# Kernel tuning notes

Hardware: AMD Instinct MI355X
Metric: run time of the kernel (lower is better)

## Reference

```python
import jax, jax.numpy as jnp
import numpy as np

B, S, D, H = 4, 2048, 512, 8
NEG_INF = -1e9


def setup_inputs() -> dict:
    key = jax.random.key(0)
    ks = jax.random.split(key, 5)
    x = jax.random.normal(ks[0], (B, S, D), dtype=jnp.float32)
    mask = jnp.ones((B, S), dtype=jnp.int32)
    sc = 0.04  # ~1/sqrt(D) init scale
    Wq = jax.random.normal(ks[1], (H, D, D), dtype=jnp.float32) * sc
    Wk = jax.random.normal(ks[2], (H, D, D), dtype=jnp.float32) * sc
    Wv = jax.random.normal(ks[3], (H, D, D), dtype=jnp.float32) * sc
    Wp = jax.random.normal(ks[4], (D, H * D), dtype=jnp.float32) * sc
    return {"x": x, "mask": mask, "Wq": Wq, "Wk": Wk, "Wv": Wv, "Wp": Wp}


def reference(x, mask, Wq, Wk, Wv, Wp):
    d = x.shape[-1]
    scale = 1.0 / jnp.sqrt(jnp.asarray(d, dtype=jnp.float32))
    # torch Linear: y = x @ W.T ; per-head full-width projections
    q = jnp.einsum("bsd,hed->bhse", x, Wq)  # [B,H,S,D]
    k = jnp.einsum("bsd,hed->bhse", x, Wk)
    v = jnp.einsum("bsd,hed->bhse", x, Wv)
    logits = jnp.einsum("bhse,bhte->bhst", q, k) * scale  # [B,H,S,S]
    # pairwise mask = outer product mask[:,:,None] @ mask[:,None,:]
    pair = (mask[:, :, None] * mask[:, None, :])[:, None, :, :]  # [B,1,S,S]
    logits = jnp.where(pair > 0, logits, NEG_INF)
    attn = jax.nn.softmax(logits, axis=-1)
    out = jnp.einsum("bhst,bhte->bhse", attn, v)  # [B,H,S,D]
    # concat heads along last dim (head order preserved) then proj (no bias)
    bsz, h, s, dd = out.shape
    cat = jnp.transpose(out, (0, 2, 1, 3)).reshape(bsz, s, h * dd)
    return jnp.einsum("bsf,df->bsd", cat, Wp)
```

## Files before the change

### kernel.cpp

```cpp
#include <hip/hip_runtime.h>
#include <hip/hip_bf16.h>


using bf16x8 = __attribute__((ext_vector_type(8))) short;
using f32x4  = __attribute__((ext_vector_type(4))) float;
typedef unsigned short u16;

__device__ __forceinline__ u16 f2bf(float f) {
  union { float f; unsigned u; } c; c.f = f;
  unsigned r = c.u + 0x7fffu + ((c.u >> 16) & 1u);
  return (u16)(r >> 16);
}

__device__ __forceinline__ void gload16(const void* g, void* l) {
  __builtin_amdgcn_global_load_lds((const __attribute__((address_space(1))) unsigned int*)g,
                                   (__attribute__((address_space(3))) unsigned int*)l, 16, 0, 0);
}

__global__ void k_cvt(const float* __restrict__ s, u16* __restrict__ d, int n4) {
  int i = blockIdx.x * 256 + threadIdx.x;
  if (i >= n4) return;
  float4 v = reinterpret_cast<const float4*>(s)[i];
  ushort4 o;
  o.x = f2bf(v.x); o.y = f2bf(v.y); o.z = f2bf(v.z); o.w = f2bf(v.w);
  reinterpret_cast<ushort4*>(d)[i] = o;
}

__global__ __launch_bounds__(256) void k_gemm_qkv(
    const u16* __restrict__ xb, const u16* __restrict__ w,
    u16* __restrict__ Qc, u16* __restrict__ Kc, u16* __restrict__ VTc,
    int h0, int HC)
{
  __shared__ u16 As[128][32];
  __shared__ u16 Bs[128][32];

  const int m0 = blockIdx.x * 128;
  const int n0 = blockIdx.y * 128;
  const int zz = blockIdx.z;
  const int t  = zz / HC, hr = zz % HC;
  const int h  = h0 + hr;

  const int tid  = threadIdx.x;
  const int lane = tid & 63, wv = tid >> 6;
  const int wr = (wv >> 1) * 64, wc = (wv & 1) * 64;
  const int r16 = lane & 15, kg = lane >> 4;

  const u16* wbase = w + (size_t)(t * 8 + h) * 512 * 512;
  const int strow = tid >> 2;
  const int sc4   = (tid & 3) * 8;

  const u16* gaa = xb    + (size_t)(m0 + strow) * 512 + sc4;
  const u16* gbb = wbase + (size_t)(n0 + strow) * 512 + sc4;
  char* AsB = (char*)&As[0][0] + wv * 1024;
  char* BsB = (char*)&Bs[0][0] + wv * 1024;

  f32x4 acc[4][4];
  f32x4 zero = {0.f, 0.f, 0.f, 0.f};
#pragma unroll
  for (int i = 0; i < 4; ++i)
#pragma unroll
    for (int j = 0; j < 4; ++j) acc[i][j] = zero;

  for (int kt = 0; kt < 16; ++kt) {
    __syncthreads();
    const int ko = kt * 32;
    gload16(gaa + ko,            AsB);
    gload16(gaa + 64 * 512 + ko, AsB + 4096);
    gload16(gbb + ko,            BsB);
    gload16(gbb + 64 * 512 + ko, BsB + 4096);
    __syncthreads();
    bf16x8 af[4], bfv[4];
#pragma unroll
    for (int i = 0; i < 4; ++i) af[i]  = *(const bf16x8*)&As[wr + i * 16 + r16][kg * 8];
#pragma unroll
    for (int j = 0; j < 4; ++j) bfv[j] = *(const bf16x8*)&Bs[wc + j * 16 + r16][kg * 8];
#pragma unroll
    for (int i = 0; i < 4; ++i)
#pragma unroll
      for (int j = 0; j < 4; ++j)
        acc[i][j] = __builtin_amdgcn_mfma_f32_16x16x32_bf16(af[i], bfv[j], acc[i][j], 0, 0, 0);
  }

#pragma unroll
  for (int i = 0; i < 4; ++i) {
    const int mbase = m0 + wr + i * 16 + kg * 4;
    const int b   = mbase >> 11;
    const int sl  = mbase & 2047;
    const int bhc = b * HC + hr;
#pragma unroll
    for (int j = 0; j < 4; ++j) {
      const int col = n0 + wc + j * 16 + r16;
      if (t == 2) {
        ushort4 o;
        o.x = f2bf(acc[i][j][0]); o.y = f2bf(acc[i][j][1]);
        o.z = f2bf(acc[i][j][2]); o.w = f2bf(acc[i][j][3]);
        *(ushort4*)&VTc[((size_t)bhc * 512 + col) * 2048 + sl] = o;
      } else if (t == 1) {
#pragma unroll
        for (int q = 0; q < 4; ++q) {
          const int s   = sl + q;
          const int row = s & 63;
          const size_t idx = ((size_t)bhc << 20)
                           + (size_t)((s >> 6) * 4 + (col >> 7)) * 8192
                           + row * 128 + ((col & 127) ^ ((row & 7) << 3));
          Kc[idx] = f2bf(acc[i][j][q]);
        }
      } else {
#pragma unroll
        for (int q = 0; q < 4; ++q)
          Qc[((size_t)bhc * 2048 + sl + q) * 512 + col] = f2bf(acc[i][j][q]);
      }
    }
  }
}

__global__ __launch_bounds__(256) void k_attn(
    const u16* __restrict__ Qc, const u16* __restrict__ Kc, const u16* __restrict__ VTc,
    const int* __restrict__ mask, u16* __restrict__ catc, int HC)
{
  __shared__ u16  Qs[32 * 512];
  __shared__ u16  Ks[2 * 8192];
  __shared__ float S_lds[32][68];
  __shared__ u16  P_lds[32][72];
  __shared__ float m_run[32], l_run[32], alpha_s[32];

  const int lin = blockIdx.x + (blockIdx.y << 6);
  int qt, bhc;
  if (HC >= 2) {
    const int pxb  = HC >> 1;
    const int slot = lin >> 3;
    bhc = (lin & 7) * pxb + (slot >> 6);
    qt  = slot & 63;
  } else {
    qt = lin & 63; bhc = lin >> 6;
  }

  const int b = bhc / HC, hr = bhc % HC;
  const int q0 = qt * 32;

  const int tid = threadIdx.x, lane = tid & 63, wv = tid >> 6;
  const int r16 = lane & 15, kg = lane >> 4;

  const u16* Qg = Qc + ((size_t)bhc * 2048 + q0) * 512;
  const u16* Kg = Kc + ((size_t)bhc << 20);
  const u16* Vg = VTc + (size_t)bhc * 512 * 2048;
  const int* mrow = mask + b * 2048;

  for (int s = tid; s < 2048; s += 256) {
    const int row = s >> 6, col = (s & 63) * 8;
    *(int4*)&Qs[row * 512 + (col ^ ((row & 7) << 3))] =
        *(const int4*)(Qg + row * 512 + col);
  }
  if (tid < 32) { m_run[tid] = -__builtin_inff(); l_run[tid] = 0.f; }

  auto kissue = [&](int gi, int cur) {
    const u16* g = Kg + (size_t)gi * 8192 + wv * 2048 + lane * 8;
    u16* l = &Ks[cur * 8192 + wv * 2048];
#pragma unroll
    for (int r = 0; r < 4; ++r)
      gload16(g + r * 512, l + r * 512);
  };

  kissue(0, 0);
  kissue(1, 1);

  asm volatile("s_waitcnt lgkmcnt(0)" ::: "memory");
  __builtin_amdgcn_s_barrier();

  const int sm_row = tid >> 3, sm_c0 = (tid & 7) * 8;
  const int rm = mrow[q0 + sm_row];
  const int krow = wv * 16 + r16;
  const int kswz = (krow & 7) << 3;

  f32x4 acc[2][8];
  f32x4 zero = {0.f, 0.f, 0.f, 0.f};
#pragma unroll
  for (int mi = 0; mi < 2; ++mi)
#pragma unroll
    for (int nf = 0; nf < 8; ++nf) acc[mi][nf] = zero;

  const float scale = 0.044194173824159216f;

  for (int it = 0; it < 32; ++it) {
    const int t0 = it * 64;
    f32x4 sacc[2] = {zero, zero};

#pragma unroll
    for (int c = 0; c < 4; ++c) {
      const int gi = it * 4 + c;
      const int cur = gi & 1;
      asm volatile("s_waitcnt vmcnt(4)" ::: "memory");
      __builtin_amdgcn_s_setprio(1);
#pragma unroll
      for (int ks = 0; ks < 4; ++ks) {
        bf16x8 kb = *(const bf16x8*)&Ks[cur * 8192 + krow * 128 + ((ks * 32 + kg * 8) ^ kswz)];
#pragma unroll
        for (int mi = 0; mi < 2; ++mi) {
          const int qrow = mi * 16 + r16;
          bf16x8 qa = *(const bf16x8*)&Qs[qrow * 512 +
              ((c * 128 + ks * 32 + kg * 8) ^ ((qrow & 7) << 3))];
          sacc[mi] = __builtin_amdgcn_mfma_f32_16x16x32_bf16(qa, kb, sacc[mi], 0, 0, 0);
        }
      }
      __builtin_amdgcn_s_setprio(0);
      if (c == 3) {
#pragma unroll
        for (int mi = 0; mi < 2; ++mi)
#pragma unroll
          for (int q = 0; q < 4; ++q)
            S_lds[mi * 16 + kg * 4 + q][wv * 16 + r16] = sacc[mi][q];
      }
      asm volatile("s_waitcnt lgkmcnt(0)" ::: "memory");
      __builtin_amdgcn_sched_barrier(0);
      if (gi + 2 < 128) kissue(gi + 2, cur);
    }
    __builtin_amdgcn_s_barrier();

    bf16x8 vfrag[2][8];
#pragma unroll
    for (int ks = 0; ks < 2; ++ks)
#pragma unroll
      for (int nf = 0; nf < 8; ++nf)
        vfrag[ks][nf] = *(const bf16x8*)(Vg +
            (size_t)(wv * 128 + nf * 16 + r16) * 2048 + t0 + ks * 32 + kg * 8);

    {
      float4 sA = *(float4*)&S_lds[sm_row][sm_c0];
      float4 sB = *(float4*)&S_lds[sm_row][sm_c0 + 4];
      const int4 cA = *(const int4*)(mrow + t0 + sm_c0);
      const int4 cB = *(const int4*)(mrow + t0 + sm_c0 + 4);
      float s0 = (rm && cA.x) ? sA.x * scale : -1e9f;
      float s1 = (rm && cA.y) ? sA.y * scale : -1e9f;
      float s2 = (rm && cA.z) ? sA.z * scale : -1e9f;
      float s3 = (rm && cA.w) ? sA.w * scale : -1e9f;
      float s4 = (rm && cB.x) ? sB.x * scale : -1e9f;
      float s5 = (rm && cB.y) ? sB.y * scale : -1e9f;
      float s6 = (rm && cB.z) ? sB.z * scale : -1e9f;
      float s7 = (rm && cB.w) ? sB.w * scale : -1e9f;
      float mt = fmaxf(fmaxf(fmaxf(s0, s1), fmaxf(s2, s3)),
                       fmaxf(fmaxf(s4, s5), fmaxf(s6, s7)));
      mt = fmaxf(mt, __shfl_xor(mt, 1));
      mt = fmaxf(mt, __shfl_xor(mt, 2));
      mt = fmaxf(mt, __shfl_xor(mt, 4));
      const float mo = m_run[sm_row];
      const float mn = fmaxf(mo, mt);
      const float al = __expf(mo - mn);
      float p0 = __expf(s0 - mn), p1 = __expf(s1 - mn);
      float p2 = __expf(s2 - mn), p3 = __expf(s3 - mn);
      float p4 = __expf(s4 - mn), p5 = __expf(s5 - mn);
      float p6 = __expf(s6 - mn), p7 = __expf(s7 - mn);
      float ps = ((p0 + p1) + (p2 + p3)) + ((p4 + p5) + (p6 + p7));
      ps += __shfl_xor(ps, 1); ps += __shfl_xor(ps, 2); ps += __shfl_xor(ps, 4);
      ushort4 w0, w1;
      w0.x = f2bf(p0); w0.y = f2bf(p1); w0.z = f2bf(p2); w0.w = f2bf(p3);
      w1.x = f2bf(p4); w1.y = f2bf(p5); w1.z = f2bf(p6); w1.w = f2bf(p7);
      *(ushort4*)&P_lds[sm_row][sm_c0]     = w0;
      *(ushort4*)&P_lds[sm_row][sm_c0 + 4] = w1;
      if ((tid & 7) == 0) {
        m_run[sm_row] = mn;
        l_run[sm_row] = l_run[sm_row] * al + ps;
        alpha_s[sm_row] = al;
      }
    }
    asm volatile("s_waitcnt lgkmcnt(0)" ::: "memory");
    __builtin_amdgcn_s_barrier();

    float alq[2][4];
#pragma unroll
    for (int mi = 0; mi < 2; ++mi)
#pragma unroll
      for (int q = 0; q < 4; ++q) alq[mi][q] = alpha_s[mi * 16 + kg * 4 + q];
#pragma unroll
    for (int mi = 0; mi < 2; ++mi)
#pragma unroll
      for (int nf = 0; nf < 8; ++nf) {
        acc[mi][nf][0] *= alq[mi][0]; acc[mi][nf][1] *= alq[mi][1];
        acc[mi][nf][2] *= alq[mi][2]; acc[mi][nf][3] *= alq[mi][3];
      }
    __builtin_amdgcn_s_setprio(1);
#pragma unroll
    for (int ks = 0; ks < 2; ++ks) {
      bf16x8 pa0 = *(const bf16x8*)&P_lds[r16][ks * 32 + kg * 8];
      bf16x8 pa1 = *(const bf16x8*)&P_lds[16 + r16][ks * 32 + kg * 8];
#pragma unroll
      for (int nf = 0; nf < 8; ++nf) {
        acc[0][nf] = __builtin_amdgcn_mfma_f32_16x16x32_bf16(pa0, vfrag[ks][nf], acc[0][nf], 0, 0, 0);
        acc[1][nf] = __builtin_amdgcn_mfma_f32_16x16x32_bf16(pa1, vfrag[ks][nf], acc[1][nf], 0, 0, 0);
      }
    }
    __builtin_amdgcn_s_setprio(0);
  }

  float rinv[2][4];
#pragma unroll
  for (int mi = 0; mi < 2; ++mi)
#pragma unroll
    for (int q = 0; q < 4; ++q) rinv[mi][q] = 1.0f / l_run[mi * 16 + kg * 4 + q];
  const int ldc = HC * 512;
#pragma unroll
  for (int mi = 0; mi < 2; ++mi)
#pragma unroll
    for (int nf = 0; nf < 8; ++nf) {
      const int col = hr * 512 + wv * 128 + nf * 16 + r16;
#pragma unroll
      for (int q = 0; q < 4; ++q) {
        const int row = b * 2048 + q0 + mi * 16 + kg * 4 + q;
        catc[(size_t)row * ldc + col] = f2bf(acc[mi][nf][q] * rinv[mi][q]);
      }
    }
}

__global__ __launch_bounds__(256) void k_gemm_out_sk(
    const u16* __restrict__ A, const u16* __restrict__ Bw, float* __restrict__ partial)
{
  __shared__ u16 As[128][32];
  __shared__ u16 Bs[128][32];

  const int m0 = blockIdx.x * 128;
  const int n0 = blockIdx.y * 128;
  const int z  = blockIdx.z;
  const int tid = threadIdx.x, lane = tid & 63, wv = tid >> 6;
  const int wr = (wv >> 1) * 64, wc = (wv & 1) * 64;
  const int r16 = lane & 15, kg = lane >> 4;
  const int strow = tid >> 2, sc4 = (tid & 3) * 8;

  const u16* gaa = A  + (size_t)(m0 + strow) * 4096 + z * 1024 + sc4;
  const u16* gbb = Bw + (size_t)(n0 + strow) * 4096 + z * 1024 + sc4;
  char* AsB = (char*)&As[0][0] + wv * 1024;
  char* BsB = (char*)&Bs[0][0] + wv * 1024;

  f32x4 acc[4][4];
  f32x4 zero = {0.f, 0.f, 0.f, 0.f};
#pragma unroll
  for (int i = 0; i < 4; ++i)
#pragma unroll
    for (int j = 0; j < 4; ++j) acc[i][j] = zero;

  for (int kt = 0; kt < 32; ++kt) {
    __syncthreads();
    const int ko = kt * 32;
    gload16(gaa + ko,                     AsB);
    gload16(gaa + (size_t)64 * 4096 + ko, AsB + 4096);
    gload16(gbb + ko,                     BsB);
    gload16(gbb + (size_t)64 * 4096 + ko, BsB + 4096);
    __syncthreads();
    bf16x8 af[4], bfv[4];
#pragma unroll
    for (int i = 0; i < 4; ++i) af[i]  = *(const bf16x8*)&As[wr + i * 16 + r16][kg * 8];
#pragma unroll
    for (int j = 0; j < 4; ++j) bfv[j] = *(const bf16x8*)&Bs[wc + j * 16 + r16][kg * 8];
#pragma unroll
    for (int i = 0; i < 4; ++i)
#pragma unroll
      for (int j = 0; j < 4; ++j)
        acc[i][j] = __builtin_amdgcn_mfma_f32_16x16x32_bf16(af[i], bfv[j], acc[i][j], 0, 0, 0);
  }

  float* dst = partial + (size_t)z * 4194304;
#pragma unroll
  for (int i = 0; i < 4; ++i)
#pragma unroll
    for (int j = 0; j < 4; ++j) {
      const int col = n0 + wc + j * 16 + r16;
#pragma unroll
      for (int q = 0; q < 4; ++q) {
        const int row = m0 + wr + i * 16 + kg * 4 + q;
        dst[(size_t)row * 512 + col] = acc[i][j][q];
      }
    }
}

__global__ void k_red4(const float* __restrict__ p, float* __restrict__ out, int n4) {
  int i = blockIdx.x * 256 + threadIdx.x;
  if (i >= n4) return;
  float4 a = reinterpret_cast<const float4*>(p)[i];
  float4 b = reinterpret_cast<const float4*>(p + 4194304)[i];
  float4 c = reinterpret_cast<const float4*>(p + 8388608)[i];
  float4 d = reinterpret_cast<const float4*>(p + 12582912)[i];
  float4 o;
  o.x = (a.x + b.x) + (c.x + d.x);
  o.y = (a.y + b.y) + (c.y + d.y);
  o.z = (a.z + b.z) + (c.z + d.z);
  o.w = (a.w + b.w) + (c.w + d.w);
  reinterpret_cast<float4*>(out)[i] = o;
}

__global__ __launch_bounds__(256) void k_gemm_out(
    const u16* __restrict__ A, const u16* __restrict__ Bw, float* __restrict__ out,
    int HC, int h0, int init)
{
  __shared__ u16 As[128][32];
  __shared__ u16 Bs[128][32];

  const int m0 = blockIdx.x * 128;
  const int n0 = blockIdx.y * 128;
  const int tid = threadIdx.x, lane = tid & 63, wv = tid >> 6;
  const int wr = (wv >> 1) * 64, wc = (wv & 1) * 64;
  const int r16 = lane & 15, kg = lane >> 4;
  const int strow = tid >> 2, sc4 = (tid & 3) * 8;
  const size_t lda = (size_t)HC * 512;
  const int nkt = HC * 16;

  const u16* gaa = A  + (size_t)(m0 + strow) * lda + sc4;
  const u16* gbb = Bw + (size_t)(n0 + strow) * 4096 + h0 * 512 + sc4;
  char* AsB = (char*)&As[0][0] + wv * 1024;
  char* BsB = (char*)&Bs[0][0] + wv * 1024;

  f32x4 acc[4][4];
  f32x4 zero = {0.f, 0.f, 0.f, 0.f};
#pragma unroll
  for (int i = 0; i < 4; ++i)
#pragma unroll
    for (int j = 0; j < 4; ++j) acc[i][j] = zero;

  for (int kt = 0; kt < nkt; ++kt) {
    __syncthreads();
    const int ko = kt * 32;
    gload16(gaa + ko,            AsB);
    gload16(gaa + 64 * lda + ko, AsB + 4096);
    gload16(gbb + ko,            BsB);
    gload16(gbb + (size_t)64 * 4096 + ko, BsB + 4096);
    __syncthreads();
    bf16x8 af[4], bfv[4];
#pragma unroll
    for (int i = 0; i < 4; ++i) af[i]  = *(const bf16x8*)&As[wr + i * 16 + r16][kg * 8];
#pragma unroll
    for (int j = 0; j < 4; ++j) bfv[j] = *(const bf16x8*)&Bs[wc + j * 16 + r16][kg * 8];
#pragma unroll
    for (int i = 0; i < 4; ++i)
#pragma unroll
      for (int j = 0; j < 4; ++j)
        acc[i][j] = __builtin_amdgcn_mfma_f32_16x16x32_bf16(af[i], bfv[j], acc[i][j], 0, 0, 0);
  }

#pragma unroll
  for (int i = 0; i < 4; ++i)
#pragma unroll
    for (int j = 0; j < 4; ++j) {
      const int col = n0 + wc + j * 16 + r16;
#pragma unroll
      for (int q = 0; q < 4; ++q) {
        const int row = m0 + wr + i * 16 + kg * 4 + q;
        if (init) out[(size_t)row * 512 + col] = acc[i][j][q];
        else      out[(size_t)row * 512 + col] += acc[i][j][q];
      }
    }
}

extern "C" void kernel_launch(void* const* d_in, const int* in_sizes, int n_in,
                              void* d_out, int out_size, void* d_ws, size_t ws_size,
                              hipStream_t stream)
{
  (void)in_sizes; (void)n_in; (void)out_size;
  const float* x  = (const float*)d_in[0];
  const int* mask = (const int*)d_in[1];
  const float* Wq = (const float*)d_in[2];
  const float* Wk = (const float*)d_in[3];
  const float* Wv = (const float*)d_in[4];
  const float* Wp = (const float*)d_in[5];

  const size_t MiB = 1024 * 1024;
  int HC = 1;
  if (ws_size >= 24 * MiB + 32 * 8 * MiB)      HC = 8;
  else if (ws_size >= 24 * MiB + 32 * 4 * MiB) HC = 4;
  else if (ws_size >= 24 * MiB + 32 * 2 * MiB) HC = 2;

  char* ws = (char*)d_ws;
  size_t off = 0;
  u16* xb   = (u16*)(ws + off); off += 8 * MiB;
  u16* wqkv = (u16*)(ws + off); off += 12 * MiB;
  u16* wpb  = (u16*)(ws + off); off += 4 * MiB;
  const size_t qsz = (size_t)4 * HC * 2048 * 512 * 2;
  u16* Qc  = (u16*)(ws + off); off += qsz;
  u16* Kc  = (u16*)(ws + off); off += qsz;
  u16* VTc = (u16*)(ws + off); off += qsz;
  u16* catc = (u16*)(ws + off);

  k_cvt<<<4096, 256, 0, stream>>>(x,  xb, 1048576);
  k_cvt<<<2048, 256, 0, stream>>>(Wq, wqkv,           524288);
  k_cvt<<<2048, 256, 0, stream>>>(Wk, wqkv + 2097152, 524288);
  k_cvt<<<2048, 256, 0, stream>>>(Wv, wqkv + 4194304, 524288);
  k_cvt<<<2048, 256, 0, stream>>>(Wp, wpb,            524288);

  for (int h0 = 0; h0 < 8; h0 += HC) {
    k_gemm_qkv<<<dim3(64, 4, 3 * HC), 256, 0, stream>>>(xb, wqkv, Qc, Kc, VTc, h0, HC);
    k_attn<<<dim3(64, 4 * HC), 256, 0, stream>>>(Qc, Kc, VTc, mask, catc, HC);
    if (HC == 8) {
      k_gemm_out_sk<<<dim3(64, 4, 4), 256, 0, stream>>>(catc, wpb, (float*)Qc);
      k_red4<<<4096, 256, 0, stream>>>((const float*)Qc, (float*)d_out, 1048576);
    } else {
      k_gemm_out<<<dim3(64, 4), 256, 0, stream>>>(catc, wpb, (float*)d_out, HC, h0, h0 == 0);
    }
  }
}
```

Baseline: 1.381 ms.

## Store V in fragment-major layout, halve K tiles, bitmask mask, reuse S buffer for P

```diff
diff --git a/kernel.cpp b/kernel.cpp
--- a/kernel.cpp
+++ b/kernel.cpp
@@ -28,7 +28,7 @@
 
 __global__ __launch_bounds__(256) void k_gemm_qkv(
     const u16* __restrict__ xb, const u16* __restrict__ w,
-    u16* __restrict__ Qc, u16* __restrict__ Kc, u16* __restrict__ VTc,
+    u16* __restrict__ Qc, u16* __restrict__ Kc, u16* __restrict__ VF,
     int h0, int HC)
 {
   __shared__ u16 As[128][32];
@@ -91,18 +91,21 @@
     for (int j = 0; j < 4; ++j) {
       const int col = n0 + wc + j * 16 + r16;
       if (t == 2) {
+        const size_t base =
+            ((((size_t)(bhc * 32 + (sl >> 6)) * 4 + (col >> 7)) * 2 + ((sl >> 5) & 1)) * 8
+             + ((col >> 4) & 7)) * 64;
+        const size_t idx = (base + ((sl >> 3) & 3) * 16 + (col & 15)) * 8 + (sl & 7);
         ushort4 o;
         o.x = f2bf(acc[i][j][0]); o.y = f2bf(acc[i][j][1]);
         o.z = f2bf(acc[i][j][2]); o.w = f2bf(acc[i][j][3]);
-        *(ushort4*)&VTc[((size_t)bhc * 512 + col) * 2048 + sl] = o;
+        *(ushort4*)&VF[idx] = o;
       } else if (t == 1) {
 #pragma unroll
         for (int q = 0; q < 4; ++q) {
-          const int s   = sl + q;
-          const int row = s & 63;
+          const int s = sl + q;
           const size_t idx = ((size_t)bhc << 20)
-                           + (size_t)((s >> 6) * 4 + (col >> 7)) * 8192
-                           + row * 128 + ((col & 127) ^ ((row & 7) << 3));
+                           + (size_t)((s >> 6) * 8 + (col >> 6)) * 4096
+                           + (s & 63) * 64 + ((col & 63) ^ ((s & 7) << 3));
           Kc[idx] = f2bf(acc[i][j][q]);
         }
       } else {
@@ -115,13 +118,13 @@
 }
 
 __global__ __launch_bounds__(256) void k_attn(
-    const u16* __restrict__ Qc, const u16* __restrict__ Kc, const u16* __restrict__ VTc,
+    const u16* __restrict__ Qc, const u16* __restrict__ Kc, const u16* __restrict__ VF,
     const int* __restrict__ mask, u16* __restrict__ catc, int HC)
 {
   __shared__ u16  Qs[32 * 512];
-  __shared__ u16  Ks[2 * 8192];
+  __shared__ u16  Ks[2 * 4096];
   __shared__ float S_lds[32][68];
-  __shared__ u16  P_lds[32][72];
+  __shared__ unsigned long long Mb[32];
   __shared__ float m_run[32], l_run[32], alpha_s[32];
 
   const int lin = blockIdx.x + (blockIdx.y << 6);
@@ -143,7 +146,7 @@
 
   const u16* Qg = Qc + ((size_t)bhc * 2048 + q0) * 512;
   const u16* Kg = Kc + ((size_t)bhc << 20);
-  const u16* Vg = VTc + (size_t)bhc * 512 * 2048;
+  const u16* Vg = VF + ((size_t)bhc << 20);
   const int* mrow = mask + b * 2048;
 
   for (int s = tid; s < 2048; s += 256) {
@@ -151,14 +154,19 @@
     *(int4*)&Qs[row * 512 + (col ^ ((row & 7) << 3))] =
         *(const int4*)(Qg + row * 512 + col);
   }
+#pragma unroll
+  for (int r = 0; r < 8; ++r) {
+    const int c = r * 256 + wv * 64 + lane;
+    unsigned long long bm = __ballot(mrow[c] != 0);
+    if (lane == 0) Mb[r * 4 + wv] = bm;
+  }
   if (tid < 32) { m_run[tid] = -__builtin_inff(); l_run[tid] = 0.f; }
 
   auto kissue = [&](int gi, int cur) {
-    const u16* g = Kg + (size_t)gi * 8192 + wv * 2048 + lane * 8;
-    u16* l = &Ks[cur * 8192 + wv * 2048];
-#pragma unroll
-    for (int r = 0; r < 4; ++r)
-      gload16(g + r * 512, l + r * 512);
+    const u16* g = Kg + (size_t)gi * 4096 + wv * 1024 + lane * 8;
+    u16* l = &Ks[cur * 4096 + wv * 1024];
+    gload16(g, l);
+    gload16(g + 512, l + 512);
   };
 
   kissue(0, 0);
@@ -182,28 +190,27 @@
   const float scale = 0.044194173824159216f;
 
   for (int it = 0; it < 32; ++it) {
-    const int t0 = it * 64;
     f32x4 sacc[2] = {zero, zero};
 
 #pragma unroll
-    for (int c = 0; c < 4; ++c) {
-      const int gi = it * 4 + c;
+    for (int c = 0; c < 8; ++c) {
+      const int gi = it * 8 + c;
       const int cur = gi & 1;
-      asm volatile("s_waitcnt vmcnt(4)" ::: "memory");
+      asm volatile("s_waitcnt vmcnt(2)" ::: "memory");
       __builtin_amdgcn_s_setprio(1);
 #pragma unroll
-      for (int ks = 0; ks < 4; ++ks) {
-        bf16x8 kb = *(const bf16x8*)&Ks[cur * 8192 + krow * 128 + ((ks * 32 + kg * 8) ^ kswz)];
+      for (int ks = 0; ks < 2; ++ks) {
+        bf16x8 kb = *(const bf16x8*)&Ks[cur * 4096 + krow * 64 + ((ks * 32 + kg * 8) ^ kswz)];
 #pragma unroll
         for (int mi = 0; mi < 2; ++mi) {
           const int qrow = mi * 16 + r16;
           bf16x8 qa = *(const bf16x8*)&Qs[qrow * 512 +
-              ((c * 128 + ks * 32 + kg * 8) ^ ((qrow & 7) << 3))];
+              ((c * 64 + ks * 32 + kg * 8) ^ ((qrow & 7) << 3))];
           sacc[mi] = __builtin_amdgcn_mfma_f32_16x16x32_bf16(qa, kb, sacc[mi], 0, 0, 0);
         }
       }
       __builtin_amdgcn_s_setprio(0);
-      if (c == 3) {
+      if (c == 7) {
 #pragma unroll
         for (int mi = 0; mi < 2; ++mi)
 #pragma unroll
@@ -212,7 +219,7 @@
       }
       asm volatile("s_waitcnt lgkmcnt(0)" ::: "memory");
       __builtin_amdgcn_sched_barrier(0);
-      if (gi + 2 < 128) kissue(gi + 2, cur);
+      if (gi + 2 < 256) kissue(gi + 2, cur);
     }
     __builtin_amdgcn_s_barrier();
 
@@ -222,21 +229,20 @@
 #pragma unroll
       for (int nf = 0; nf < 8; ++nf)
         vfrag[ks][nf] = *(const bf16x8*)(Vg +
-            (size_t)(wv * 128 + nf * 16 + r16) * 2048 + t0 + ks * 32 + kg * 8);
+            ((((size_t)it * 4 + wv) * 2 + ks) * 8 + nf) * 512 + (size_t)lane * 8);
 
     {
       float4 sA = *(float4*)&S_lds[sm_row][sm_c0];
       float4 sB = *(float4*)&S_lds[sm_row][sm_c0 + 4];
-      const int4 cA = *(const int4*)(mrow + t0 + sm_c0);
-      const int4 cB = *(const int4*)(mrow + t0 + sm_c0 + 4);
-      float s0 = (rm && cA.x) ? sA.x * scale : -1e9f;
-      float s1 = (rm && cA.y) ? sA.y * scale : -1e9f;
-      float s2 = (rm && cA.z) ? sA.z * scale : -1e9f;
-      float s3 = (rm && cA.w) ? sA.w * scale : -1e9f;
-      float s4 = (rm && cB.x) ? sB.x * scale : -1e9f;
-      float s5 = (rm && cB.y) ? sB.y * scale : -1e9f;
-      float s6 = (rm && cB.z) ? sB.z * scale : -1e9f;
-      float s7 = (rm && cB.w) ? sB.w * scale : -1e9f;
+      const unsigned byte = rm ? (unsigned)((Mb[it] >> sm_c0) & 0xFF) : 0u;
+      float s0 = (byte & 1)   ? sA.x * scale : -1e9f;
+      float s1 = (byte & 2)   ? sA.y * scale : -1e9f;
+      float s2 = (byte & 4)   ? sA.z * scale : -1e9f;
+      float s3 = (byte & 8)   ? sA.w * scale : -1e9f;
+      float s4 = (byte & 16)  ? sB.x * scale : -1e9f;
+      float s5 = (byte & 32)  ? sB.y * scale : -1e9f;
+      float s6 = (byte & 64)  ? sB.z * scale : -1e9f;
+      float s7 = (byte & 128) ? sB.w * scale : -1e9f;
       float mt = fmaxf(fmaxf(fmaxf(s0, s1), fmaxf(s2, s3)),
                        fmaxf(fmaxf(s4, s5), fmaxf(s6, s7)));
       mt = fmaxf(mt, __shfl_xor(mt, 1));
@@ -254,8 +260,9 @@
       ushort4 w0, w1;
       w0.x = f2bf(p0); w0.y = f2bf(p1); w0.z = f2bf(p2); w0.w = f2bf(p3);
       w1.x = f2bf(p4); w1.y = f2bf(p5); w1.z = f2bf(p6); w1.w = f2bf(p7);
-      *(ushort4*)&P_lds[sm_row][sm_c0]     = w0;
-      *(ushort4*)&P_lds[sm_row][sm_c0 + 4] = w1;
+      u16* Pcell = (u16*)&S_lds[sm_row][sm_c0];
+      *(ushort4*)(Pcell)     = w0;
+      *(ushort4*)(Pcell + 4) = w1;
       if ((tid & 7) == 0) {
         m_run[sm_row] = mn;
         l_run[sm_row] = l_run[sm_row] * al + ps;
@@ -280,8 +287,8 @@
     __builtin_amdgcn_s_setprio(1);
 #pragma unroll
     for (int ks = 0; ks < 2; ++ks) {
-      bf16x8 pa0 = *(const bf16x8*)&P_lds[r16][ks * 32 + kg * 8];
-      bf16x8 pa1 = *(const bf16x8*)&P_lds[16 + r16][ks * 32 + kg * 8];
+      bf16x8 pa0 = *(const bf16x8*)((const u16*)&S_lds[r16][0]      + (ks * 32 + kg * 8) * 2);
+      bf16x8 pa1 = *(const bf16x8*)((const u16*)&S_lds[16 + r16][0] + (ks * 32 + kg * 8) * 2);
 #pragma unroll
       for (int nf = 0; nf < 8; ++nf) {
         acc[0][nf] = __builtin_amdgcn_mfma_f32_16x16x32_bf16(pa0, vfrag[ks][nf], acc[0][nf], 0, 0, 0);
@@ -289,6 +296,8 @@
       }
     }
     __builtin_amdgcn_s_setprio(0);
+    asm volatile("s_waitcnt lgkmcnt(0)" ::: "memory");
+    __builtin_amdgcn_s_barrier();
   }
 
   float rinv[2][4];
@@ -473,7 +482,7 @@
   const size_t qsz = (size_t)4 * HC * 2048 * 512 * 2;
   u16* Qc  = (u16*)(ws + off); off += qsz;
   u16* Kc  = (u16*)(ws + off); off += qsz;
-  u16* VTc = (u16*)(ws + off); off += qsz;
+  u16* VF  = (u16*)(ws + off); off += qsz;
   u16* catc = (u16*)(ws + off);
 
   k_cvt<<<4096, 256, 0, stream>>>(x,  xb, 1048576);
@@ -483,8 +492,8 @@
   k_cvt<<<2048, 256, 0, stream>>>(Wp, wpb,            524288);
 
   for (int h0 = 0; h0 < 8; h0 += HC) {
-    k_gemm_qkv<<<dim3(64, 4, 3 * HC), 256, 0, stream>>>(xb, wqkv, Qc, Kc, VTc, h0, HC);
-    k_attn<<<dim3(64, 4 * HC), 256, 0, stream>>>(Qc, Kc, VTc, mask, catc, HC);
+    k_gemm_qkv<<<dim3(64, 4, 3 * HC), 256, 0, stream>>>(xb, wqkv, Qc, Kc, VF, h0, HC);
+    k_attn<<<dim3(64, 4 * HC), 256, 0, stream>>>(Qc, Kc, VF, mask, catc, HC);
     if (HC == 8) {
       k_gemm_out_sk<<<dim3(64, 4, 4), 256, 0, stream>>>(catc, wpb, (float*)Qc);
       k_red4<<<4096, 256, 0, stream>>>((const float*)Qc, (float*)d_out, 1048576);
```

Result: faster. 1.255 ms (-9.1%).
